# Optimization experiments

Hardware: AMD Instinct MI355X
Metric: run time of the kernel (lower is better)

## Reference

```python
import jax, jax.numpy as jnp
import numpy as np

H = 32        # hiddenSize
OUT = 256     # output_size
T = 60        # num_frames
EPS = 1e-5


def setup_inputs() -> dict:
    key = jax.random.key(0)
    ks = jax.random.split(key, 16)
    s = 0.05
    rn = lambda k, shp: (jax.random.normal(k, shp, dtype=jnp.float32) * s)
    return {
        "x": jax.random.normal(ks[0], (1, T, 63), dtype=jnp.float32),
        "w00": rn(ks[1], (63, 63)), "b00": rn(ks[2], (63,)),
        "w01": rn(ks[3], (64, 63)), "b01": rn(ks[4], (64,)),
        "ln_g": jnp.ones((64,), jnp.float32), "ln_b": jnp.zeros((64,), jnp.float32),
        "w_ih": rn(ks[5], (4 * H, 64)), "w_hh": rn(ks[6], (4 * H, H)),
        "b_ih": rn(ks[7], (4 * H,)), "b_hh": rn(ks[8], (4 * H,)),
        "bn_g": jnp.ones((H,), jnp.float32), "bn_b": jnp.zeros((H,), jnp.float32),
        "w10": rn(ks[9], (32, H)), "b10": rn(ks[10], (32,)),
        "w11": rn(ks[11], (32, 32)), "b11": rn(ks[12], (32,)),
        "w12": rn(ks[13], (OUT, 32)), "b12": rn(ks[14], (OUT,)),
    }


def _forward(x, w00, b00, w01, b01, ln_g, ln_b, w_ih, w_hh, b_ih, b_hh,
             bn_g, bn_b, w10, b10, w11, b11, w12, b12):
    # x: [1, T, 63] -> scan over T frames (fused MLP + LayerNorm + LSTM cell)
    xs = jnp.transpose(x, (1, 0, 2))  # [T, 1, 63]

    def step(carry, xt):  # xt: [1, 63]
        h, c = carry
        f = jax.nn.relu(xt @ w00.T + b00)          # [1, 63]
        f = jax.nn.relu(f @ w01.T + b01)           # [1, 64]
        mu = jnp.mean(f, axis=-1, keepdims=True)
        var = jnp.mean((f - mu) ** 2, axis=-1, keepdims=True)
        f = (f - mu) * jax.lax.rsqrt(var + EPS) * ln_g + ln_b
        gates = f @ w_ih.T + b_ih + h @ w_hh.T + b_hh  # [1, 4H]
        i_g, f_g, g_g, o_g = jnp.split(gates, 4, axis=-1)
        c = jax.nn.sigmoid(f_g) * c + jax.nn.sigmoid(i_g) * jnp.tanh(g_g)
        h = jax.nn.sigmoid(o_g) * jnp.tanh(c)
        return (h, c), None

    h0 = jnp.zeros((1, H), x.dtype)
    c0 = jnp.zeros((1, H), x.dtype)
    (h, _), _ = jax.lax.scan(step, (h0, c0), xs)
    # BatchNorm1d in eval mode (running_mean=0, running_var=1)
    out = h * jax.lax.rsqrt(jnp.float32(1.0) + EPS) * bn_g + bn_b
    out = jax.nn.relu(out @ w10.T + b10)
    out = jax.nn.relu(out @ w11.T + b11)
    return out @ w12.T + b12  # [1, OUT]


def reference(x, w00, b00, w01, b01, ln_g, ln_b, w_ih, w_hh, b_ih, b_hh,
              bn_g, bn_b, w10, b10, w11, b11, w12, b12):
    return _forward(x, w00, b00, w01, b01, ln_g, ln_b, w_ih, w_hh, b_ih, b_hh,
                    bn_g, bn_b, w10, b10, w11, b11, w12, b12)
```

## Files before the change

### kernel.cpp

```cpp
#include <hip/hip_runtime.h>

#define EPS 1e-5f
#define MAGIC 0x5CA9F1A6u

typedef __fp16 h2v2 __attribute__((ext_vector_type(2)));

__device__ __forceinline__ float frcp(float x) { return __builtin_amdgcn_rcpf(x); }
__device__ __forceinline__ float fsigm(float x) { return frcp(1.0f + __expf(-x)); }
__device__ __forceinline__ float ftanh(float x) {
    float e = __expf(-2.0f * x);
    return (1.0f - e) * frcp(1.0f + e);
}
__device__ __forceinline__ int rdli(int v, int k) {
    return __builtin_amdgcn_readlane(v, k);
}
__device__ __forceinline__ float rdl32(float v, int k) {
    return __int_as_float(__builtin_amdgcn_readlane(__float_as_int(v), 32 + k));
}
__device__ __forceinline__ float xhalf_sum(float x) {
#if __has_builtin(__builtin_amdgcn_permlane32_swap)
    auto r = __builtin_amdgcn_permlane32_swap(__float_as_uint(x),
                                              __float_as_uint(x), false, false);
    return __uint_as_float(r[0]) + __uint_as_float(r[1]);
#else
    return x + __shfl_xor(x, 32);
#endif
}
__device__ __forceinline__ float fdot2(h2v2 a, h2v2 b, float c) {
#if __has_builtin(__builtin_amdgcn_fdot2)
    return __builtin_amdgcn_fdot2(a, b, c, false);
#else
    return c + (float)a.x * (float)b.x + (float)a.y * (float)b.y;
#endif
}

__global__ __launch_bounds__(64) void fused_kernel(
    const float* __restrict__ x,
    const float* __restrict__ w00, const float* __restrict__ b00,
    const float* __restrict__ w01, const float* __restrict__ b01,
    const float* __restrict__ ln_g, const float* __restrict__ ln_b,
    const float* __restrict__ w_ih, const float* __restrict__ w_hh,
    const float* __restrict__ b_ih, const float* __restrict__ b_hh,
    const float* __restrict__ bn_g, const float* __restrict__ bn_b,
    const float* __restrict__ w10, const float* __restrict__ b10,
    const float* __restrict__ w11, const float* __restrict__ b11,
    const float* __restrict__ w12, const float* __restrict__ b12,
    float* __restrict__ Gx, unsigned* __restrict__ flags,
    float* __restrict__ out)
{
    __shared__ float smem[16324];
    const int j = threadIdx.x;

    if (blockIdx.x < 60) {
        const int t = blockIdx.x;
        float* w00s = smem;
        float* w01s = smem + 3972;
        float* wihT = smem + 8004;
        float* scr  = smem + 16196;

        {
            const float4* g4 = (const float4*)w00;
            float4* s4 = (float4*)w00s;
            for (int i = j; i < 992; i += 64) s4[i] = g4[i];
            if (j == 0) w00s[3968] = w00[3968];
        }
        {
            const float4* g4 = (const float4*)w01;
            float4* s4 = (float4*)w01s;
            for (int i = j; i < 1008; i += 64) s4[i] = g4[i];
        }
        for (int r = j; r < 128; r += 64) {
            const float4* row = (const float4*)(w_ih + r * 64);
            #pragma unroll
            for (int q = 0; q < 16; q++) {
                float4 v = row[q];
                wihT[(4 * q + 0) * 128 + r] = v.x;
                wihT[(4 * q + 1) * 128 + r] = v.y;
                wihT[(4 * q + 2) * 128 + r] = v.z;
                wihT[(4 * q + 3) * 128 + r] = v.w;
            }
        }
        scr[j] = (j < 63) ? x[t * 63 + j] : 0.0f;
        __syncthreads();

        float f0 = 0.0f;
        if (j < 63) {
            float acc = b00[j];
            const float* wr = w00s + j * 63;
            #pragma unroll
            for (int k = 0; k < 63; k++) acc += scr[k] * wr[k];
            f0 = fmaxf(acc, 0.0f);
        }
        __syncthreads();
        scr[j] = f0;
        __syncthreads();

        float acc = b01[j];
        {
            const float* wr = w01s + j * 63;
            #pragma unroll
            for (int k = 0; k < 63; k++) acc += scr[k] * wr[k];
        }
        float f1 = fmaxf(acc, 0.0f);

        float s = f1, sq = f1 * f1;
        #pragma unroll
        for (int off = 32; off > 0; off >>= 1) {
            s  += __shfl_xor(s, off);
            sq += __shfl_xor(sq, off);
        }
        float mu  = s * (1.0f / 64.0f);
        float var = sq * (1.0f / 64.0f) - mu * mu;
        float f   = (f1 - mu) * rsqrtf(var + EPS) * ln_g[j] + ln_b[j];
        __syncthreads();
        scr[64 + j] = f;
        __syncthreads();

        float a0 = b_ih[j] + b_hh[j];
        float a1 = b_ih[j + 64] + b_hh[j + 64];
        #pragma unroll
        for (int k = 0; k < 64; k++) {
            float fk = scr[64 + k];
            a0 += fk * wihT[k * 128 + j];
            a1 += fk * wihT[k * 128 + 64 + j];
        }
        Gx[t * 128 + j]      = a0;
        Gx[t * 128 + 64 + j] = a1;

        __threadfence();
        __syncthreads();
        if (j == 0)
            __hip_atomic_store(&flags[t], MAGIC, __ATOMIC_RELEASE,
                               __HIP_MEMORY_SCOPE_AGENT);
        return;
    }

    float* gxs = smem;

    h2v2 wAh[16], wBh[16];
    {
        const float4* r0 = (const float4*)(w_hh + j * 32);
        const float4* r1 = (const float4*)(w_hh + (j + 64) * 32);
        #pragma unroll
        for (int q = 0; q < 8; q++) {
            float4 a = r0[q];
            float4 b = r1[q];
            wAh[2 * q + 0] = __builtin_amdgcn_cvt_pkrtz(a.x, a.y);
            wAh[2 * q + 1] = __builtin_amdgcn_cvt_pkrtz(a.z, a.w);
            wBh[2 * q + 0] = __builtin_amdgcn_cvt_pkrtz(b.x, b.y);
            wBh[2 * q + 1] = __builtin_amdgcn_cvt_pkrtz(b.z, b.w);
        }
    }

    {
        bool done = (j >= 60);
        while (true) {
            if (!done)
                done = (__hip_atomic_load(&flags[j], __ATOMIC_RELAXED,
                                          __HIP_MEMORY_SCOPE_AGENT) == MAGIC);
            if (__ballot(done) == ~0ULL) break;
            __builtin_amdgcn_s_sleep(1);
        }
        (void)__hip_atomic_load(&flags[0], __ATOMIC_ACQUIRE,
                                __HIP_MEMORY_SCOPE_AGENT);
    }

    {
        const float4* g4 = (const float4*)Gx;
        float4* s4 = (float4*)gxs;
        for (int i = j; i < 1920; i += 64) s4[i] = g4[i];
    }
    __syncthreads();

    const bool low = (j < 32);
    float c = 0.0f, hn = 0.0f;
    #pragma unroll 1
    for (int c0 = 0; c0 < 5; c0++) {
        float gAr[12], gBr[12];
        #pragma unroll
        for (int i = 0; i < 12; i++) {
            gAr[i] = gxs[(c0 * 12 + i) * 128 + j];
            gBr[i] = gxs[(c0 * 12 + i) * 128 + 64 + j];
        }
        #pragma unroll
        for (int i = 0; i < 12; i++) {
            int   hsw_i = __builtin_amdgcn_update_dpp(
                              0, __float_as_int(hn), 0xB1, 0xF, 0xF, true);
            h2v2  hpk   = __builtin_amdgcn_cvt_pkrtz(hn, __int_as_float(hsw_i));
            int   hpk_i = __builtin_bit_cast(int, hpk);

            int hh_i[16];
            #pragma unroll
            for (int k = 0; k < 16; k++) hh_i[k] = rdli(hpk_i, 32 + 2 * k);

            float aA0 = gAr[i], aA1 = 0.f, aA2 = 0.f, aA3 = 0.f;
            float aB0 = gBr[i], aB1 = 0.f, aB2 = 0.f, aB3 = 0.f;
            #pragma unroll
            for (int d = 0; d < 4; d++) {
                h2v2 h0 = __builtin_bit_cast(h2v2, hh_i[d]);
                h2v2 h1 = __builtin_bit_cast(h2v2, hh_i[4 + d]);
                h2v2 hx = __builtin_bit_cast(h2v2, hh_i[8 + d]);
                h2v2 h3 = __builtin_bit_cast(h2v2, hh_i[12 + d]);
                aA0 = fdot2(h0, wAh[d],      aA0);  aB0 = fdot2(h0, wBh[d],      aB0);
                aA1 = fdot2(h1, wAh[4 + d],  aA1);  aB1 = fdot2(h1, wBh[4 + d],  aB1);
                aA2 = fdot2(hx, wAh[8 + d],  aA2);  aB2 = fdot2(hx, wBh[8 + d],  aB2);
                aA3 = fdot2(h3, wAh[12 + d], aA3);  aB3 = fdot2(h3, wBh[12 + d], aB3);
            }
            float a0 = (aA0 + aA1) + (aA2 + aA3);
            float a1 = (aB0 + aB1) + (aB2 + aB3);

            float e1 = __expf(-a1);
            float sO = frcp(1.0f + e1);
            float e2 = e1 * e1;
            float t1 = (1.0f - e2) * frcp(1.0f + e2);
            float s0 = fsigm(a0);
            float own = s0 * (low ? t1 : c);
            c = xhalf_sum(own);
            hn = sO * ftanh(c);
        }
    }

    const float rs = rsqrtf(1.0f + EPS);
    const int ro = j & 31;
    float acc = b10[ro];
    #pragma unroll
    for (int k = 0; k < 32; k++) {
        float hkk = rdl32(hn, k);
        float hb = hkk * rs * bn_g[k] + bn_b[k];
        acc += w10[ro * 32 + k] * hb;
    }
    float o1 = fmaxf(acc, 0.0f);

    acc = b11[ro];
    #pragma unroll
    for (int k = 0; k < 32; k++)
        acc += w11[ro * 32 + k]
             * __int_as_float(__builtin_amdgcn_readlane(__float_as_int(o1), k));
    float o2 = fmaxf(acc, 0.0f);

    float a[4];
    #pragma unroll
    for (int r = 0; r < 4; r++) a[r] = b12[j + 64 * r];
    #pragma unroll
    for (int k = 0; k < 32; k++) {
        float hv = __int_as_float(__builtin_amdgcn_readlane(__float_as_int(o2), k));
        #pragma unroll
        for (int r = 0; r < 4; r++) a[r] += w12[(j + 64 * r) * 32 + k] * hv;
    }
    #pragma unroll
    for (int r = 0; r < 4; r++) out[j + 64 * r] = a[r];
}

extern "C" void kernel_launch(void* const* d_in, const int* in_sizes, int n_in,
                              void* d_out, int out_size, void* d_ws, size_t ws_size,
                              hipStream_t stream) {
    const float* x    = (const float*)d_in[0];
    const float* w00  = (const float*)d_in[1];
    const float* b00  = (const float*)d_in[2];
    const float* w01  = (const float*)d_in[3];
    const float* b01  = (const float*)d_in[4];
    const float* ln_g = (const float*)d_in[5];
    const float* ln_b = (const float*)d_in[6];
    const float* w_ih = (const float*)d_in[7];
    const float* w_hh = (const float*)d_in[8];
    const float* b_ih = (const float*)d_in[9];
    const float* b_hh = (const float*)d_in[10];
    const float* bn_g = (const float*)d_in[11];
    const float* bn_b = (const float*)d_in[12];
    const float* w10  = (const float*)d_in[13];
    const float* b10  = (const float*)d_in[14];
    const float* w11  = (const float*)d_in[15];
    const float* b11  = (const float*)d_in[16];
    const float* w12  = (const float*)d_in[17];
    const float* b12  = (const float*)d_in[18];
    float* out = (float*)d_out;
    float*    Gx    = (float*)d_ws;
    unsigned* flags = (unsigned*)((char*)d_ws + 49152);

    fused_kernel<<<61, 64, 0, stream>>>(x, w00, b00, w01, b01, ln_g, ln_b,
                                        w_ih, w_hh, b_ih, b_hh, bn_g, bn_b,
                                        w10, b10, w11, b11, w12, b12,
                                        Gx, flags, out);
}
```

Baseline: 124.3 us.

## Read weights and Gx directly from global memory instead of staging in LDS

The producer blocks no longer copy w00, w01 and a transposed w_ih into shared memory. They read the weight rows straight from global memory (L1/L2), which removes about 64KB of LDS per block plus the staging copies and transposes. The recurrent block now loads the precomputed Gx from global memory on each chunk rather than bulk-copying it into LDS first. The cost is uncoalesced per-thread row reads (stride 63/64 floats) and global-latency loads inside the serial LSTM chunk loop.

```diff
diff --git a/kernel.cpp b/kernel.cpp
--- a/kernel.cpp
+++ b/kernel.cpp
@@ -48,45 +48,19 @@
     float* __restrict__ Gx, unsigned* __restrict__ flags,
     float* __restrict__ out)
 {
-    __shared__ float smem[16324];
+    __shared__ float scr[128];
     const int j = threadIdx.x;
 
     if (blockIdx.x < 60) {
         const int t = blockIdx.x;
-        float* w00s = smem;
-        float* w01s = smem + 3972;
-        float* wihT = smem + 8004;
-        float* scr  = smem + 16196;
-
-        {
-            const float4* g4 = (const float4*)w00;
-            float4* s4 = (float4*)w00s;
-            for (int i = j; i < 992; i += 64) s4[i] = g4[i];
-            if (j == 0) w00s[3968] = w00[3968];
-        }
-        {
-            const float4* g4 = (const float4*)w01;
-            float4* s4 = (float4*)w01s;
-            for (int i = j; i < 1008; i += 64) s4[i] = g4[i];
-        }
-        for (int r = j; r < 128; r += 64) {
-            const float4* row = (const float4*)(w_ih + r * 64);
-            #pragma unroll
-            for (int q = 0; q < 16; q++) {
-                float4 v = row[q];
-                wihT[(4 * q + 0) * 128 + r] = v.x;
-                wihT[(4 * q + 1) * 128 + r] = v.y;
-                wihT[(4 * q + 2) * 128 + r] = v.z;
-                wihT[(4 * q + 3) * 128 + r] = v.w;
-            }
-        }
+
         scr[j] = (j < 63) ? x[t * 63 + j] : 0.0f;
         __syncthreads();
 
         float f0 = 0.0f;
         if (j < 63) {
+            const float* wr = w00 + j * 63;
             float acc = b00[j];
-            const float* wr = w00s + j * 63;
             #pragma unroll
             for (int k = 0; k < 63; k++) acc += scr[k] * wr[k];
             f0 = fmaxf(acc, 0.0f);
@@ -97,7 +71,7 @@
 
         float acc = b01[j];
         {
-            const float* wr = w01s + j * 63;
+            const float* wr = w01 + j * 63;
             #pragma unroll
             for (int k = 0; k < 63; k++) acc += scr[k] * wr[k];
         }
@@ -118,11 +92,13 @@
 
         float a0 = b_ih[j] + b_hh[j];
         float a1 = b_ih[j + 64] + b_hh[j + 64];
+        const float* wi0 = w_ih + j * 64;
+        const float* wi1 = w_ih + (j + 64) * 64;
         #pragma unroll
         for (int k = 0; k < 64; k++) {
             float fk = scr[64 + k];
-            a0 += fk * wihT[k * 128 + j];
-            a1 += fk * wihT[k * 128 + 64 + j];
+            a0 += fk * wi0[k];
+            a1 += fk * wi1[k];
         }
         Gx[t * 128 + j]      = a0;
         Gx[t * 128 + 64 + j] = a1;
@@ -134,8 +110,6 @@
                                __HIP_MEMORY_SCOPE_AGENT);
         return;
     }
-
-    float* gxs = smem;
 
     h2v2 wAh[16], wBh[16];
     {
@@ -165,13 +139,6 @@
                                 __HIP_MEMORY_SCOPE_AGENT);
     }
 
-    {
-        const float4* g4 = (const float4*)Gx;
-        float4* s4 = (float4*)gxs;
-        for (int i = j; i < 1920; i += 64) s4[i] = g4[i];
-    }
-    __syncthreads();
-
     const bool low = (j < 32);
     float c = 0.0f, hn = 0.0f;
     #pragma unroll 1
@@ -179,8 +146,8 @@
         float gAr[12], gBr[12];
         #pragma unroll
         for (int i = 0; i < 12; i++) {
-            gAr[i] = gxs[(c0 * 12 + i) * 128 + j];
-            gBr[i] = gxs[(c0 * 12 + i) * 128 + 64 + j];
+            gAr[i] = Gx[(c0 * 12 + i) * 128 + j];
+            gBr[i] = Gx[(c0 * 12 + i) * 128 + 64 + j];
         }
         #pragma unroll
         for (int i = 0; i < 12; i++) {
```

Result: faster. 109.0 us, median of 2 (-12.3%).
